# Kernel tuning notes

Measured on AMD Instinct MI355X. Metric: run time of the kernel, lower is better.

## Reference

```python
import jax, jax.numpy as jnp
import numpy as np

B, NNEG, D, E = 16384, 10, 8, 64
N_ENT = 500000  # sum(domain_dims.values())
N_PAIRS = D * (D - 1) // 2


def setup_inputs() -> dict:
    key = jax.random.key(0)
    k1, k2, k3, k4, k5 = jax.random.split(key, 5)
    return {
        "pos_x": jax.random.randint(k1, (B, D), 0, N_ENT, dtype=jnp.int32),
        "neg_x": jax.random.randint(k2, (B, NNEG, D), 0, N_ENT, dtype=jnp.int32),
        "emb_table": jax.random.normal(k3, (N_ENT, E), dtype=jnp.float32) * 0.01,
        "pair_w": jax.random.uniform(k4, (N_PAIRS,), dtype=jnp.float32),
        "c": jax.random.uniform(k5, (1,), dtype=jnp.float32),
    }


def _obtain_score(x, emb_table, pair_w, c):
    # x: [..., D] int indices into the shared embedding table
    e = emb_table[x]                                   # [..., D, E] gather
    gram = jnp.einsum('...de,...fe->...df', e, e)      # [..., D, D] pairwise dots
    iu, ju = np.triu_indices(D, k=1)
    pair_dots = gram[..., iu, ju]                      # [..., N_PAIRS]
    # NOTE: the original torch code never increments k inside obtain_score,
    # so EVERY pair is scaled by exp(pair_W['0']). We replicate that faithfully.
    r = pair_dots * jnp.exp(pair_w[0])
    return jnp.exp(jnp.sum(r, axis=-1) + c[0])         # [...]


def reference(pos_x, neg_x, emb_table, pair_w, c):
    pos_score = _obtain_score(pos_x, emb_table, pair_w, c)   # [B]
    # vectorized over the negative-sample axis (original loops in Python)
    neg_score = _obtain_score(neg_x, emb_table, pair_w, c)   # [B, NNEG]
    return pos_score, neg_score
```

## Files before the change

### kernel.cpp

```cpp
#include <hip/hip_runtime.h>
#include <cstdint>

constexpr int B     = 16384;
constexpr int NNEG  = 10;
constexpr int D     = 8;
constexpr int E     = 64;
constexpr int ROWS  = B * (1 + NNEG);
constexpr int RPW   = 4;
constexpr int WPB   = 4;
constexpr int LDS_PER_WAVE = D * 1024;

__device__ __forceinline__ void dma16(const float* gp, void* lp) {
    __builtin_amdgcn_global_load_lds(
        (const __attribute__((address_space(1))) void*)gp,
        (__attribute__((address_space(3))) void*)lp,
        16, 0, 0);
}

__global__ __launch_bounds__(256) void APE_61555471286335_kernel(
    const int*   __restrict__ pos_x,
    const int*   __restrict__ neg_x,
    const float* __restrict__ emb,
    const float* __restrict__ pair_w,
    const float* __restrict__ c,
    float*       __restrict__ out)
{
    __shared__ char smem[WPB * LDS_PER_WAVE];

    const int lane = threadIdx.x & 63;
    const int wid  = threadIdx.x >> 6;
    const int wave = blockIdx.x * WPB + wid;
    const int g    = lane >> 4;
    const int t    = lane & 15;
    const int row  = wave * RPW + g;

    char* base = smem + wid * LDS_PER_WAVE;

    const int* idx = (row < B) ? (pos_x + (size_t)row * D)
                               : (neg_x + (size_t)(row - B) * D);
    const int4 i0 = *(const int4*)(idx);
    const int4 i1 = *(const int4*)(idx + 4);
    const int id[D] = {i0.x, i0.y, i0.z, i0.w, i1.x, i1.y, i1.z, i1.w};

#pragma unroll
    for (int d = 0; d < D; ++d) {
        const float* gp = emb + (size_t)id[d] * E + t * 4;
        dma16(gp, base + d * 1024 + lane * 16);
    }

    __builtin_amdgcn_s_waitcnt(0x0f70);
    __syncthreads();

    float4 s = make_float4(0.f, 0.f, 0.f, 0.f), q = s;
#pragma unroll
    for (int d = 0; d < D; ++d) {
        const float4 v = *(const float4*)(base + d * 1024 + lane * 16);
        s.x += v.x; s.y += v.y; s.z += v.z; s.w += v.w;
        q.x += v.x * v.x; q.y += v.y * v.y;
        q.z += v.z * v.z; q.w += v.w * v.w;
    }
    float p = s.x * s.x + s.y * s.y + s.z * s.z + s.w * s.w
            - (q.x + q.y + q.z + q.w);

#pragma unroll
    for (int off = 8; off > 0; off >>= 1)
        p += __shfl_xor(p, off, 64);

    if (t == 0) {
        out[row] = expf(0.5f * p * expf(pair_w[0]) + c[0]);
    }
}

extern "C" void kernel_launch(void* const* d_in, const int* in_sizes, int n_in,
                              void* d_out, int out_size, void* d_ws, size_t ws_size,
                              hipStream_t stream) {
    const int*   pos_x  = (const int*)  d_in[0];
    const int*   neg_x  = (const int*)  d_in[1];
    const float* emb    = (const float*)d_in[2];
    const float* pair_w = (const float*)d_in[3];
    const float* c      = (const float*)d_in[4];
    float*       out    = (float*)      d_out;

    constexpr int BLOCK = 256;
    constexpr int ROWS_PER_BLOCK = WPB * RPW;
    static_assert(ROWS % ROWS_PER_BLOCK == 0, "exact grid");
    const int grid = ROWS / ROWS_PER_BLOCK;

    APE_61555471286335_kernel<<<grid, BLOCK, 0, stream>>>(
        pos_x, neg_x, emb, pair_w, c, out);
}
```

Baseline: 212.5 us.

## Double-buffer LDS gathers across four row batches per wave

Each wave now handles four batches of rows. The gather DMA for the next batch is issued into a second LDS buffer while the current batch is reduced, with vmcnt waits instead of a block-wide barrier. Blocks shrink to two waves and the scalar scale and offset are hoisted out of the loop. This is meant to hide gather latency inside a wave, at the cost of fewer waves in the grid and more LDS per wave, which could lower occupancy-based latency hiding.

```diff
diff --git a/kernel.cpp b/kernel.cpp
--- a/kernel.cpp
+++ b/kernel.cpp
@@ -7,8 +7,12 @@
 constexpr int E     = 64;
 constexpr int ROWS  = B * (1 + NNEG);
 constexpr int RPW   = 4;
-constexpr int WPB   = 4;
-constexpr int LDS_PER_WAVE = D * 1024;
+constexpr int NB    = 4;
+constexpr int WPB   = 2;
+constexpr int BATCH_BYTES    = D * 1024;
+constexpr int LDS_PER_WAVE   = 2 * BATCH_BYTES;
+constexpr int ROWS_PER_WAVE  = RPW * NB;
+constexpr int ROWS_PER_BLOCK = WPB * ROWS_PER_WAVE;
 
 __device__ __forceinline__ void dma16(const float* gp, void* lp) {
     __builtin_amdgcn_global_load_lds(
@@ -17,7 +21,7 @@
         16, 0, 0);
 }
 
-__global__ __launch_bounds__(256) void APE_61555471286335_kernel(
+__global__ __launch_bounds__(128) void APE_61555471286335_kernel(
     const int*   __restrict__ pos_x,
     const int*   __restrict__ neg_x,
     const float* __restrict__ emb,
@@ -32,42 +36,63 @@
     const int wave = blockIdx.x * WPB + wid;
     const int g    = lane >> 4;
     const int t    = lane & 15;
-    const int row  = wave * RPW + g;
+    const int rowBase = wave * ROWS_PER_WAVE + g;
 
     char* base = smem + wid * LDS_PER_WAVE;
 
-    const int* idx = (row < B) ? (pos_x + (size_t)row * D)
-                               : (neg_x + (size_t)(row - B) * D);
-    const int4 i0 = *(const int4*)(idx);
-    const int4 i1 = *(const int4*)(idx + 4);
-    const int id[D] = {i0.x, i0.y, i0.z, i0.w, i1.x, i1.y, i1.z, i1.w};
+    int id[NB][D];
+#pragma unroll
+    for (int k = 0; k < NB; ++k) {
+        const int row = rowBase + k * RPW;
+        const int* ip = (row < B) ? (pos_x + (size_t)row * D)
+                                  : (neg_x + (size_t)(row - B) * D);
+        const int4 a = ((const int4*)ip)[0];
+        const int4 b = ((const int4*)ip)[1];
+        id[k][0] = a.x; id[k][1] = a.y; id[k][2] = a.z; id[k][3] = a.w;
+        id[k][4] = b.x; id[k][5] = b.y; id[k][6] = b.z; id[k][7] = b.w;
+    }
+
+    float sc = expf(pair_w[0]);
+    float c0 = c[0];
+    asm volatile("" : "+v"(sc), "+v"(c0));
 
 #pragma unroll
-    for (int d = 0; d < D; ++d) {
-        const float* gp = emb + (size_t)id[d] * E + t * 4;
-        dma16(gp, base + d * 1024 + lane * 16);
-    }
-
-    __builtin_amdgcn_s_waitcnt(0x0f70);
-    __syncthreads();
-
-    float4 s = make_float4(0.f, 0.f, 0.f, 0.f), q = s;
-#pragma unroll
-    for (int d = 0; d < D; ++d) {
-        const float4 v = *(const float4*)(base + d * 1024 + lane * 16);
-        s.x += v.x; s.y += v.y; s.z += v.z; s.w += v.w;
-        q.x += v.x * v.x; q.y += v.y * v.y;
-        q.z += v.z * v.z; q.w += v.w * v.w;
-    }
-    float p = s.x * s.x + s.y * s.y + s.z * s.z + s.w * s.w
-            - (q.x + q.y + q.z + q.w);
+    for (int d = 0; d < D; ++d)
+        dma16(emb + (size_t)id[0][d] * E + t * 4,
+              base + d * 1024 + lane * 16);
 
 #pragma unroll
-    for (int off = 8; off > 0; off >>= 1)
-        p += __shfl_xor(p, off, 64);
+    for (int k = 0; k < NB; ++k) {
+        if (k + 1 < NB) {
+            char* nbuf = base + ((k + 1) & 1) * BATCH_BYTES;
+#pragma unroll
+            for (int d = 0; d < D; ++d)
+                dma16(emb + (size_t)id[k + 1][d] * E + t * 4,
+                      nbuf + d * 1024 + lane * 16);
+            __builtin_amdgcn_s_waitcnt(0x0f78);
+        } else {
+            __builtin_amdgcn_s_waitcnt(0x0f70);
+        }
+        asm volatile("" ::: "memory");
 
-    if (t == 0) {
-        out[row] = expf(0.5f * p * expf(pair_w[0]) + c[0]);
+        const char* bk = base + (k & 1) * BATCH_BYTES;
+        float4 s = make_float4(0.f, 0.f, 0.f, 0.f), q = s;
+#pragma unroll
+        for (int d = 0; d < D; ++d) {
+            const float4 v = *(const float4*)(bk + d * 1024 + lane * 16);
+            s.x += v.x; s.y += v.y; s.z += v.z; s.w += v.w;
+            q.x += v.x * v.x; q.y += v.y * v.y;
+            q.z += v.z * v.z; q.w += v.w * v.w;
+        }
+        float p = s.x * s.x + s.y * s.y + s.z * s.z + s.w * s.w
+                - (q.x + q.y + q.z + q.w);
+
+#pragma unroll
+        for (int off = 8; off > 0; off >>= 1)
+            p += __shfl_xor(p, off, 64);
+
+        if (t == 0)
+            out[rowBase + k * RPW] = expf(0.5f * p * sc + c0);
     }
 }
 
@@ -81,8 +106,7 @@
     const float* c      = (const float*)d_in[4];
     float*       out    = (float*)      d_out;
 
-    constexpr int BLOCK = 256;
-    constexpr int ROWS_PER_BLOCK = WPB * RPW;
+    constexpr int BLOCK = WPB * 64;
     static_assert(ROWS % ROWS_PER_BLOCK == 0, "exact grid");
     const int grid = ROWS / ROWS_PER_BLOCK;
 
```

Result: no change. 213.6 us (+0.5%).
